# Optimization experiments

Measured on AMD Instinct MI355X. Metric: run time of the kernel, lower is better.

Reference implementation:

```python
import jax, jax.numpy as jnp
import numpy as np
from jax import lax

B, T, D, R, V = 128, 8, 2048, 4, 512

def setup_inputs() -> dict:
    key = jax.random.key(0)
    k0, k1, k2, k3, k4 = jax.random.split(key, 5)
    # scales chosen so the TT products stay within fp32 range (see notes)
    input_embs = jax.random.normal(k0, (B, T, D), dtype=jnp.float32) * 0.1
    label_ids = jax.random.randint(k1, (B, T), 0, V)
    w_alpha = jax.random.normal(k2, (D, R), dtype=jnp.float32) * 0.04
    w_beta = jax.random.normal(k3, (D, R), dtype=jnp.float32) * 0.04
    w_vocab = jax.random.normal(k4, (D, V * R * R), dtype=jnp.float32) * 0.04
    return {"input_embs": input_embs, "label_ids": label_ids,
            "w_alpha": w_alpha, "w_beta": w_beta, "w_vocab": w_vocab}

def _tt_loss(input_embs, w_alpha, w_beta, w_vocab, label_ids):
    b, t, d = input_embs.shape
    flat = input_embs.reshape(-1, d)                    # [B*T, D]
    alpha = jnp.abs((flat @ w_alpha).reshape(b, t, R).mean(1))   # [B, R]
    beta = jnp.abs((flat @ w_beta).reshape(b, t, R).mean(1))     # [B, R]
    core = jnp.abs((flat @ w_vocab).reshape(b, t, R, V, R).mean(1))  # [B, R, V, R]

    # --- _select: gather per-position R x R cores and chain-multiply ---
    core_v = core.transpose(0, 2, 1, 3)                 # [B, V, R, R]
    sel = jnp.take_along_axis(core_v, label_ids[:, :, None, None], axis=1)  # [B, T, R, R]
    sel_t = jnp.swapaxes(sel, 0, 1)                     # [T, B, R, R]

    def chain(carry, m):
        return jnp.einsum('bik,bkj->bij', carry, m), None
    res, _ = lax.scan(chain, sel_t[0], sel_t[1:])       # [B, R, R]
    u = jnp.einsum('bi,bij,bj->b', alpha, res, beta)    # unnormalized probs [B]

    # --- normalization constant: marg^(T+1) contracted with alpha/beta ---
    marg = core.sum(2)                                  # [B, R, R]

    def pow_step(c, _):
        return jnp.einsum('bik,bkj->bij', c, marg), None
    zmat, _ = lax.scan(pow_step, marg, None, length=t)  # marg^(t+1)
    z = jnp.einsum('bi,bij,bj->b', alpha, zmat, beta)

    loss = -jnp.log(u / z)
    return loss.mean()

def reference(input_embs, label_ids, w_alpha, w_beta, w_vocab):
    return _tt_loss(input_embs, w_alpha, w_beta, w_vocab, label_ids)
```

## Files before the change

### kernel.cpp

```cpp
#include <hip/hip_runtime.h>
#include <math.h>

#define BB 128
#define TT 8
#define DD 2048
#define RR 4
#define VV 512

typedef __attribute__((ext_vector_type(8))) short short8;
typedef __attribute__((ext_vector_type(4))) float v4f;

__device__ __forceinline__ unsigned pack_bf16(float x, float y) {
    union { float f; unsigned u; } a, b;
    a.f = x; b.f = y;
    unsigned ua = a.u + 0x7fffu + ((a.u >> 16) & 1u);
    unsigned ub = b.u + 0x7fffu + ((b.u >> 16) & 1u);
    return (ua >> 16) | (ub & 0xffff0000u);
}

__global__ __launch_bounds__(256) void phaseA(const float* __restrict__ inp,
                                              const float* __restrict__ w_alpha,
                                              const float* __restrict__ w_beta,
                                              unsigned short* __restrict__ fmb,
                                              float* __restrict__ alphaP,
                                              float* __restrict__ betaP,
                                              float* __restrict__ marg) {
    int bid = blockIdx.x;
    int b = bid >> 1, half = bid & 1;
    int tid = threadIdx.x;
    if (bid == 0) {
#pragma unroll
        for (int e = 0; e < 8; ++e) marg[e * 256 + tid] = 0.f;
    }
    const float* base = inp + (size_t)b * TT * DD;
    float pa[4] = {0.f, 0.f, 0.f, 0.f};
    float pb[4] = {0.f, 0.f, 0.f, 0.f};
#pragma unroll
    for (int i = 0; i < 4; ++i) {
        int d = half * 1024 + i * 256 + tid;
        float s = 0.f;
#pragma unroll
        for (int t = 0; t < TT; ++t) s += base[t * DD + d];
        float v = s * (1.0f / TT);
        union { float f; unsigned u; } cv; cv.f = v;
        unsigned r = cv.u + 0x7fffu + ((cv.u >> 16) & 1u);
        fmb[b * DD + d] = (unsigned short)(r >> 16);
        float4 wa = *(const float4*)(w_alpha + d * 4);
        float4 wb = *(const float4*)(w_beta + d * 4);
        pa[0] += v * wa.x; pa[1] += v * wa.y; pa[2] += v * wa.z; pa[3] += v * wa.w;
        pb[0] += v * wb.x; pb[1] += v * wb.y; pb[2] += v * wb.z; pb[3] += v * wb.w;
    }
#pragma unroll
    for (int r = 0; r < 4; ++r) {
        for (int m = 1; m < 64; m <<= 1) {
            pa[r] += __shfl_xor(pa[r], m);
            pb[r] += __shfl_xor(pb[r], m);
        }
    }
    __shared__ float red[4][8];
    if ((tid & 63) == 0) {
        int w = tid >> 6;
#pragma unroll
        for (int r = 0; r < 4; ++r) { red[w][r] = pa[r]; red[w][4 + r] = pb[r]; }
    }
    __syncthreads();
    if (tid < 8) {
        float s = red[0][tid] + red[1][tid] + red[2][tid] + red[3][tid];
        if (tid < 4) alphaP[(half * BB + b) * 4 + tid] = s;
        else         betaP[(half * BB + b) * 4 + (tid - 4)] = s;
    }
}

__global__ __launch_bounds__(256, 4) void phaseB(const unsigned short* __restrict__ fmb,
                                                 const float* __restrict__ wv,
                                                 const int* __restrict__ labels,
                                                 float* __restrict__ marg,
                                                 float* __restrict__ sel) {
    __shared__ unsigned short Ws[2][16][136];
    __shared__ int slab[BB * TT];

    const int tid = threadIdx.x;
    const int nb = blockIdx.x;
    const int col0 = nb * 16;
    const int iblk = nb >> 7;
    const int c128 = nb & 127;

    slab[tid] = labels[tid];
    slab[tid + 256] = labels[tid + 256];
    slab[tid + 512] = labels[tid + 512];
    slab[tid + 768] = labels[tid + 768];

    const int c4 = tid & 3;
    const int kp = tid >> 2;
    const int w = tid >> 6;
    const int lane = tid & 63;
    const int m15 = lane & 15;
    const int q = lane >> 4;
    const int row0 = w * 32;

    const float* wbase = wv + (size_t)(2 * kp) * 8192 + col0 + c4 * 4;
    const unsigned short* ab0 = fmb + (row0 + m15) * DD + q * 8;
    const unsigned short* ab1 = ab0 + 16 * DD;

    v4f acc0 = {0.f, 0.f, 0.f, 0.f};
    v4f acc1 = {0.f, 0.f, 0.f, 0.f};
    short8 afr[2][2][4];
    float4 sw0, sw1;

    sw0 = *(const float4*)(wbase);
    sw1 = *(const float4*)(wbase + 8192);
#pragma unroll
    for (int ks = 0; ks < 4; ++ks) {
        afr[0][0][ks] = *(const short8*)(ab0 + ks * 32);
        afr[0][1][ks] = *(const short8*)(ab1 + ks * 32);
    }
    {
        const float* f0 = (const float*)&sw0;
        const float* f1 = (const float*)&sw1;
#pragma unroll
        for (int jj = 0; jj < 4; ++jj)
            *(unsigned*)&Ws[0][c4 * 4 + jj][2 * kp] = pack_bf16(f0[jj], f1[jj]);
    }
    __syncthreads();

#pragma unroll
    for (int c = 0; c < 16; ++c) {
        const int cur = c & 1;
        if (c < 15) {
            const float* wp = wbase + (size_t)(c + 1) * 128 * 8192;
            sw0 = *(const float4*)(wp);
            sw1 = *(const float4*)(wp + 8192);
#pragma unroll
            for (int ks = 0; ks < 4; ++ks) {
                afr[1 - cur][0][ks] = *(const short8*)(ab0 + (c + 1) * 128 + ks * 32);
                afr[1 - cur][1][ks] = *(const short8*)(ab1 + (c + 1) * 128 + ks * 32);
            }
        }
#pragma unroll
        for (int ks = 0; ks < 4; ++ks) {
            short8 bf = *(const short8*)&Ws[cur][m15][ks * 32 + q * 8];
            acc0 = __builtin_amdgcn_mfma_f32_16x16x32_bf16(afr[cur][0][ks], bf, acc0, 0, 0, 0);
            acc1 = __builtin_amdgcn_mfma_f32_16x16x32_bf16(afr[cur][1][ks], bf, acc1, 0, 0, 0);
        }
        if (c < 15) {
            const float* f0 = (const float*)&sw0;
            const float* f1 = (const float*)&sw1;
#pragma unroll
            for (int jj = 0; jj < 4; ++jj)
                *(unsigned*)&Ws[1 - cur][c4 * 4 + jj][2 * kp] = pack_bf16(f0[jj], f1[jj]);
            __syncthreads();
        }
    }

    const int v0 = c128 * 4 + (m15 >> 2);
    const int e = iblk * 4 + (m15 & 3);
    const float* a0p = (const float*)&acc0;
    const float* a1p = (const float*)&acc1;
#pragma unroll
    for (int r = 0; r < 4; ++r) {
        int ma = row0 + q * 4 + r;
        int mb = ma + 16;
        float a0 = fabsf(a0p[r]);
        float a1 = fabsf(a1p[r]);
        float s0 = a0 + __shfl_xor(a0, 4); s0 += __shfl_xor(s0, 8);
        float s1 = a1 + __shfl_xor(a1, 4); s1 += __shfl_xor(s1, 8);
        if (m15 < 4) {
            atomicAdd(&marg[ma * 16 + e], s0);
            atomicAdd(&marg[mb * 16 + e], s1);
        }
#pragma unroll
        for (int t = 0; t < TT; ++t) {
            if (slab[ma * 8 + t] == v0) sel[(ma * 8 + t) * 16 + e] = a0;
            if (slab[mb * 8 + t] == v0) sel[(mb * 8 + t) * 16 + e] = a1;
        }
    }
}

__global__ __launch_bounds__(128) void phaseD(const float* __restrict__ alphaP,
                                              const float* __restrict__ betaP,
                                              const float* __restrict__ marg,
                                              const float* __restrict__ sel,
                                              float* __restrict__ out) {
    int b = threadIdx.x;
    float alpha[4], beta[4];
#pragma unroll
    for (int r = 0; r < 4; ++r) {
        alpha[r] = fabsf(alphaP[b * 4 + r] + alphaP[512 + b * 4 + r]);
        beta[r]  = fabsf(betaP[b * 4 + r] + betaP[512 + b * 4 + r]);
    }
    const float* sb = sel + b * TT * 16;
    float res[16], tmp[16], mm[16], zm[16];
#pragma unroll
    for (int ee = 0; ee < 16; ++ee) res[ee] = sb[ee];
    for (int t = 1; t < TT; ++t) {
        const float* m = sb + t * 16;
#pragma unroll
        for (int i = 0; i < 4; ++i)
#pragma unroll
            for (int jj = 0; jj < 4; ++jj) {
                float s = 0.f;
#pragma unroll
                for (int k = 0; k < 4; ++k) s += res[i * 4 + k] * m[k * 4 + jj];
                tmp[i * 4 + jj] = s;
            }
#pragma unroll
        for (int ee = 0; ee < 16; ++ee) res[ee] = tmp[ee];
    }
#pragma unroll
    for (int ee = 0; ee < 16; ++ee) { mm[ee] = marg[b * 16 + ee]; zm[ee] = mm[ee]; }
    for (int st = 0; st < TT; ++st) {
#pragma unroll
        for (int i = 0; i < 4; ++i)
#pragma unroll
            for (int jj = 0; jj < 4; ++jj) {
                float s = 0.f;
#pragma unroll
                for (int k = 0; k < 4; ++k) s += zm[i * 4 + k] * mm[k * 4 + jj];
                tmp[i * 4 + jj] = s;
            }
#pragma unroll
        for (int ee = 0; ee < 16; ++ee) zm[ee] = tmp[ee];
    }
    float u = 0.f, z = 0.f;
#pragma unroll
    for (int i = 0; i < 4; ++i) {
#pragma unroll
        for (int jj = 0; jj < 4; ++jj) {
            u += alpha[i] * res[i * 4 + jj] * beta[jj];
            z += alpha[i] * zm[i * 4 + jj] * beta[jj];
        }
    }
    float loss = logf(z) - logf(u);
    __shared__ float red[128];
    red[b] = loss;
    __syncthreads();
    for (int off = 64; off >= 1; off >>= 1) {
        if (b < off) red[b] += red[b + off];
        __syncthreads();
    }
    if (b == 0) out[0] = red[0] * (1.0f / BB);
}

extern "C" void kernel_launch(void* const* d_in, const int* in_sizes, int n_in,
                              void* d_out, int out_size, void* d_ws, size_t ws_size,
                              hipStream_t stream) {
    const float* inp     = (const float*)d_in[0];
    const int*   labels  = (const int*)d_in[1];
    const float* w_alpha = (const float*)d_in[2];
    const float* w_beta  = (const float*)d_in[3];
    const float* wv      = (const float*)d_in[4];
    float* out = (float*)d_out;

    float* ws     = (float*)d_ws;
    float* alphaP = ws;
    float* betaP  = ws + 1024;
    float* marg   = ws + 2048;
    float* sel    = ws + 4096;
    unsigned short* fmb = (unsigned short*)(ws + 20480);

    phaseA<<<256, 256, 0, stream>>>(inp, w_alpha, w_beta, fmb, alphaP, betaP, marg);
    phaseB<<<512, 256, 0, stream>>>(fmb, wv, labels, marg, sel);
    phaseD<<<1, 128, 0, stream>>>(alphaP, betaP, marg, sel, out);
}
```

Baseline: 146.3 us.

## Restructure vocab GEMM with split-K waves and direct register B-fragment loads

The phaseB GEMM now uses 256 blocks of 512 threads, each covering 32 columns and all 128 rows. Waves split K in half and combine partial sums through shared memory, so the LDS double buffer and per-chunk barriers are gone. Each lane loads its w_vocab B fragment straight into registers as strided scalar loads, and fp32 is converted to bf16 by truncation instead of round-to-nearest. This removes LDS staging and syncs, but the scalar strided global loads may coalesce worse, and truncation slightly lowers precision.

```diff
diff --git a/kernel.cpp b/kernel.cpp
--- a/kernel.cpp
+++ b/kernel.cpp
@@ -9,14 +9,6 @@
 
 typedef __attribute__((ext_vector_type(8))) short short8;
 typedef __attribute__((ext_vector_type(4))) float v4f;
-
-__device__ __forceinline__ unsigned pack_bf16(float x, float y) {
-    union { float f; unsigned u; } a, b;
-    a.f = x; b.f = y;
-    unsigned ua = a.u + 0x7fffu + ((a.u >> 16) & 1u);
-    unsigned ub = b.u + 0x7fffu + ((b.u >> 16) & 1u);
-    return (ua >> 16) | (ub & 0xffff0000u);
-}
 
 __global__ __launch_bounds__(256) void phaseA(const float* __restrict__ inp,
                                               const float* __restrict__ w_alpha,
@@ -71,107 +63,82 @@
     }
 }
 
-__global__ __launch_bounds__(256, 4) void phaseB(const unsigned short* __restrict__ fmb,
-                                                 const float* __restrict__ wv,
-                                                 const int* __restrict__ labels,
-                                                 float* __restrict__ marg,
-                                                 float* __restrict__ sel) {
-    __shared__ unsigned short Ws[2][16][136];
+__global__ __launch_bounds__(512) void phaseB(const unsigned short* __restrict__ fmb,
+                                              const float* __restrict__ wv,
+                                              const int* __restrict__ labels,
+                                              float* __restrict__ marg,
+                                              float* __restrict__ sel) {
+    __shared__ float xch[4][4][64][4];
     __shared__ int slab[BB * TT];
 
     const int tid = threadIdx.x;
+    slab[tid] = labels[tid];
+    slab[tid + 512] = labels[tid + 512];
+
     const int nb = blockIdx.x;
-    const int col0 = nb * 16;
-    const int iblk = nb >> 7;
-    const int c128 = nb & 127;
-
-    slab[tid] = labels[tid];
-    slab[tid + 256] = labels[tid + 256];
-    slab[tid + 512] = labels[tid + 512];
-    slab[tid + 768] = labels[tid + 768];
-
-    const int c4 = tid & 3;
-    const int kp = tid >> 2;
-    const int w = tid >> 6;
-    const int lane = tid & 63;
-    const int m15 = lane & 15;
-    const int q = lane >> 4;
-    const int row0 = w * 32;
-
-    const float* wbase = wv + (size_t)(2 * kp) * 8192 + col0 + c4 * 4;
-    const unsigned short* ab0 = fmb + (row0 + m15) * DD + q * 8;
-    const unsigned short* ab1 = ab0 + 16 * DD;
-
-    v4f acc0 = {0.f, 0.f, 0.f, 0.f};
-    v4f acc1 = {0.f, 0.f, 0.f, 0.f};
-    short8 afr[2][2][4];
-    float4 sw0, sw1;
-
-    sw0 = *(const float4*)(wbase);
-    sw1 = *(const float4*)(wbase + 8192);
-#pragma unroll
-    for (int ks = 0; ks < 4; ++ks) {
-        afr[0][0][ks] = *(const short8*)(ab0 + ks * 32);
-        afr[0][1][ks] = *(const short8*)(ab1 + ks * 32);
-    }
-    {
-        const float* f0 = (const float*)&sw0;
-        const float* f1 = (const float*)&sw1;
-#pragma unroll
-        for (int jj = 0; jj < 4; ++jj)
-            *(unsigned*)&Ws[0][c4 * 4 + jj][2 * kp] = pack_bf16(f0[jj], f1[jj]);
+    const int w = tid >> 6, lane = tid & 63;
+    const int m15 = lane & 15, q = lane >> 4;
+    const int ch = w & 1;
+    const int rh = (w >> 1) & 1;
+    const int kh = w >> 2;
+    const int colg = nb * 32 + ch * 16 + m15;
+
+    v4f acc[4];
+#pragma unroll
+    for (int t = 0; t < 4; ++t) acc[t] = (v4f){0.f, 0.f, 0.f, 0.f};
+
+    const float* wvp = wv + (size_t)(kh * 1024 + q * 8) * 8192 + colg;
+    const unsigned short* ap = fmb + (size_t)(rh * 64 + m15) * DD + kh * 1024 + q * 8;
+
+#pragma unroll 2
+    for (int kc = 0; kc < 32; ++kc) {
+        float f[8];
+#pragma unroll
+        for (int j = 0; j < 8; ++j) f[j] = wvp[(size_t)j * 8192];
+        short8 bf;
+        unsigned* bu = (unsigned*)&bf;
+#pragma unroll
+        for (int p = 0; p < 4; ++p) {
+            union { float ff; unsigned u; } x0, x1;
+            x0.ff = f[2 * p]; x1.ff = f[2 * p + 1];
+            bu[p] = (x0.u >> 16) | (x1.u & 0xffff0000u);
+        }
+#pragma unroll
+        for (int tile = 0; tile < 4; ++tile) {
+            short8 af = *(const short8*)(ap + tile * 16 * DD);
+            acc[tile] = __builtin_amdgcn_mfma_f32_16x16x32_bf16(af, bf, acc[tile], 0, 0, 0);
+        }
+        wvp += (size_t)32 * 8192;
+        ap += 32;
+    }
+
+    if (kh == 1) {
+#pragma unroll
+        for (int tile = 0; tile < 4; ++tile)
+            *(v4f*)&xch[w - 4][tile][lane][0] = acc[tile];
     }
     __syncthreads();
-
-#pragma unroll
-    for (int c = 0; c < 16; ++c) {
-        const int cur = c & 1;
-        if (c < 15) {
-            const float* wp = wbase + (size_t)(c + 1) * 128 * 8192;
-            sw0 = *(const float4*)(wp);
-            sw1 = *(const float4*)(wp + 8192);
-#pragma unroll
-            for (int ks = 0; ks < 4; ++ks) {
-                afr[1 - cur][0][ks] = *(const short8*)(ab0 + (c + 1) * 128 + ks * 32);
-                afr[1 - cur][1][ks] = *(const short8*)(ab1 + (c + 1) * 128 + ks * 32);
+    if (kh == 1) return;
+#pragma unroll
+    for (int tile = 0; tile < 4; ++tile)
+        acc[tile] += *(const v4f*)&xch[w][tile][lane][0];
+
+    const int i4 = (nb >> 6) * 4;
+    const int jj = m15 & 3;
+    const int v = (nb & 63) * 8 + ch * 4 + (m15 >> 2);
+#pragma unroll
+    for (int tile = 0; tile < 4; ++tile) {
+#pragma unroll
+        for (int r = 0; r < 4; ++r) {
+            int m = rh * 64 + tile * 16 + q * 4 + r;
+            float a = fabsf(acc[tile][r]);
+            float s = a + __shfl_xor(a, 4);
+            s += __shfl_xor(s, 8);
+            if (m15 < 4) atomicAdd(&marg[m * 16 + i4 + m15], s);
+#pragma unroll
+            for (int t = 0; t < TT; ++t) {
+                if (slab[m * 8 + t] == v) sel[(m * 8 + t) * 16 + i4 + jj] = a;
             }
-        }
-#pragma unroll
-        for (int ks = 0; ks < 4; ++ks) {
-            short8 bf = *(const short8*)&Ws[cur][m15][ks * 32 + q * 8];
-            acc0 = __builtin_amdgcn_mfma_f32_16x16x32_bf16(afr[cur][0][ks], bf, acc0, 0, 0, 0);
-            acc1 = __builtin_amdgcn_mfma_f32_16x16x32_bf16(afr[cur][1][ks], bf, acc1, 0, 0, 0);
-        }
-        if (c < 15) {
-            const float* f0 = (const float*)&sw0;
-            const float* f1 = (const float*)&sw1;
-#pragma unroll
-            for (int jj = 0; jj < 4; ++jj)
-                *(unsigned*)&Ws[1 - cur][c4 * 4 + jj][2 * kp] = pack_bf16(f0[jj], f1[jj]);
-            __syncthreads();
-        }
-    }
-
-    const int v0 = c128 * 4 + (m15 >> 2);
-    const int e = iblk * 4 + (m15 & 3);
-    const float* a0p = (const float*)&acc0;
-    const float* a1p = (const float*)&acc1;
-#pragma unroll
-    for (int r = 0; r < 4; ++r) {
-        int ma = row0 + q * 4 + r;
-        int mb = ma + 16;
-        float a0 = fabsf(a0p[r]);
-        float a1 = fabsf(a1p[r]);
-        float s0 = a0 + __shfl_xor(a0, 4); s0 += __shfl_xor(s0, 8);
-        float s1 = a1 + __shfl_xor(a1, 4); s1 += __shfl_xor(s1, 8);
-        if (m15 < 4) {
-            atomicAdd(&marg[ma * 16 + e], s0);
-            atomicAdd(&marg[mb * 16 + e], s1);
-        }
-#pragma unroll
-        for (int t = 0; t < TT; ++t) {
-            if (slab[ma * 8 + t] == v0) sel[(ma * 8 + t) * 16 + e] = a0;
-            if (slab[mb * 8 + t] == v0) sel[(mb * 8 + t) * 16 + e] = a1;
         }
     }
 }
@@ -259,6 +226,6 @@
     unsigned short* fmb = (unsigned short*)(ws + 20480);
 
     phaseA<<<256, 256, 0, stream>>>(inp, w_alpha, w_beta, fmb, alphaP, betaP, marg);
-    phaseB<<<512, 256, 0, stream>>>(fmb, wv, labels, marg, sel);
+    phaseB<<<256, 512, 0, stream>>>(fmb, wv, labels, marg, sel);
     phaseD<<<1, 128, 0, stream>>>(alphaP, betaP, marg, sel, out);
 }
```

Measured after the change: 151.0 us. 1.03x slower.
